# Performance work log

Measured on AMD Instinct MI355X. Metric: run time of the kernel, lower is better.

## Reference

```python
import jax, jax.numpy as jnp
import numpy as np

B, N, F_IN, HID, OUT, NHEADS = 16, 1024, 64, 64, 64, 4
TAXI = 512        # get_Parameter('taxi_size') from the original repo (node split point)
ALPHA = 0.2       # LeakyReLU negative slope


def setup_inputs() -> dict:
    key = jax.random.key(0)
    ks = jax.random.split(key, 8)
    x = jax.random.normal(ks[0], (B, N, F_IN), dtype=jnp.float32)
    # multiplicative binary mask (mostly ones so softmax rows are well-conditioned)
    mask = (jax.random.uniform(ks[1], (N, N)) > 0.1).astype(jnp.float32)
    s_in = 1.0 / np.sqrt(F_IN)
    s_cat = 1.0 / np.sqrt(NHEADS * HID)
    W1 = jax.random.normal(ks[2], (NHEADS, F_IN, HID), jnp.float32) * s_in
    W2 = jax.random.normal(ks[3], (NHEADS, F_IN, HID), jnp.float32) * s_in
    a = jax.random.normal(ks[4], (NHEADS, 2 * HID), jnp.float32) * 0.1
    W1o = jax.random.normal(ks[5], (NHEADS * HID, OUT), jnp.float32) * s_cat
    W2o = jax.random.normal(ks[6], (NHEADS * HID, OUT), jnp.float32) * s_cat
    ao = jax.random.normal(ks[7], (2 * OUT,), jnp.float32) * 0.1
    return dict(x=x, mask=mask, W1=W1, W2=W2, a=a, W1o=W1o, W2o=W2o, ao=ao)


def _gat_layer(x, mask, W1, W2, a, out_dim):
    # x: [B,N,F]; W1,W2: [F,out_dim]; a: [2*out_dim]
    # node-group-split linear projection (taxi nodes via W1, rest via W2)
    h = jnp.concatenate([x[:, :TAXI] @ W1, x[:, TAXI:] @ W2], axis=1)  # [B,N,O]
    A1 = h @ a[:out_dim]                 # [B,N]
    A2 = h @ a[out_dim:]                 # [B,N]
    sim = A1[:, :, None] + A2[:, None, :]  # [B,N,N] additive scores
    e = jax.nn.leaky_relu(sim, ALPHA)
    e = mask[None, :, :] * e             # multiplicative mask (as in source)
    attn = jax.nn.softmax(e, axis=-1)    # [B,N,N]  (dropout omitted: eval mode)
    h_prime = jnp.einsum('bnm,bmo->bno', attn, h)
    return jax.nn.elu(h_prime), attn


def reference(x, mask, W1, W2, a, W1o, W2o, ao):
    # input dropout omitted (eval mode)
    heads = [_gat_layer(x, mask, W1[i], W2[i], a[i], HID)[0] for i in range(NHEADS)]
    xc = jnp.concatenate(heads, axis=-1)          # [B,N,NHEADS*HID]
    out, attn = _gat_layer(xc, mask, W1o, W2o, ao, OUT)
    return out, attn
```

## Files before the change

### kernel.cpp

```cpp
#include <hip/hip_runtime.h>
#include <hip/hip_bf16.h>

#define B_      16
#define N_      1024
#define ALPHA_  0.2f

typedef __attribute__((ext_vector_type(8))) __bf16 bf16x8;
typedef __attribute__((ext_vector_type(4))) __bf16 bf16x4;
typedef __attribute__((ext_vector_type(4))) float  floatx4;

__device__ __forceinline__ float eluf(float u) { return u > 0.f ? u : __expf(u) - 1.f; }

__device__ __forceinline__ floatx4 mfma_bf16(bf16x8 a, bf16x8 b, floatx4 c) {
    return __builtin_amdgcn_mfma_f32_16x16x32_bf16(a, b, c, 0, 0, 0);
}

__device__ __forceinline__ void t_quad(const float4 a2v, const float4 ep, const float4 en,
                                       const float4 mv, const float th,
                                       const float e1p, const float e1n,
                                       float& z, float* o)
{
    float t0 = ((a2v.x > th) ? ep.x : en.x) * ((a2v.x > th) ? e1p : e1n);
    float t1 = ((a2v.y > th) ? ep.y : en.y) * ((a2v.y > th) ? e1p : e1n);
    float t2 = ((a2v.z > th) ? ep.z : en.z) * ((a2v.z > th) ? e1p : e1n);
    float t3 = ((a2v.w > th) ? ep.w : en.w) * ((a2v.w > th) ? e1p : e1n);
    t0 = (mv.x != 0.f) ? t0 : 1.f;
    t1 = (mv.y != 0.f) ? t1 : 1.f;
    t2 = (mv.z != 0.f) ? t2 : 1.f;
    t3 = (mv.w != 0.f) ? t3 : 1.f;
    z += ((t0 + t1) + (t2 + t3));
    o[0] = t0; o[1] = t1; o[2] = t2; o[3] = t3;
}

__global__ __launch_bounds__(256) void proj1_kernel(
    const float* __restrict__ x, const float* __restrict__ W1,
    const float* __restrict__ W2, const float* __restrict__ av,
    __bf16* __restrict__ h1t, float* __restrict__ A1, float* __restrict__ A2)
{
    const int tile = blockIdx.x, b = blockIdx.y, head = blockIdx.z;
    const int n0 = tile * 64;
    const float* W  = ((n0 < 512) ? W1 : W2) + head * 64 * 64;
    const float* ah = av + head * 128;

    __shared__ __align__(16) __bf16 xs[64][72];
    __shared__ __align__(16) __bf16 Wt[64][72];
    __shared__ __align__(16) float as_[128];

    const int tid = threadIdx.x;
    if (tid < 128) as_[tid] = ah[tid];
#pragma unroll
    for (int i = 0; i < 4; ++i) {
        int idx = i * 256 + tid;
        int r = idx >> 4, c = (idx & 15) * 4;
        float4 v = *(const float4*)(x + ((size_t)(b * N_ + n0 + r)) * 64 + c);
        xs[r][c+0] = (__bf16)v.x; xs[r][c+1] = (__bf16)v.y;
        xs[r][c+2] = (__bf16)v.z; xs[r][c+3] = (__bf16)v.w;
        float4 wv = *(const float4*)(W + (size_t)r * 64 + c);
        Wt[c+0][r] = (__bf16)wv.x; Wt[c+1][r] = (__bf16)wv.y;
        Wt[c+2][r] = (__bf16)wv.z; Wt[c+3][r] = (__bf16)wv.w;
    }
    __syncthreads();

    const int w = tid >> 6, L = tid & 63, quad = L >> 4, lo = L & 15;
    floatx4 acc[4] = {{0,0,0,0},{0,0,0,0},{0,0,0,0},{0,0,0,0}};
#pragma unroll
    for (int kc = 0; kc < 2; ++kc) {
        bf16x8 af = *(bf16x8*)&xs[16 * w + lo][kc * 32 + quad * 8];
#pragma unroll
        for (int t = 0; t < 4; ++t) {
            bf16x8 bv = *(bf16x8*)&Wt[16 * t + lo][kc * 32 + quad * 8];
            acc[t] = mfma_bf16(af, bv, acc[t]);
        }
    }

    float p1[4] = {0, 0, 0, 0}, p2[4] = {0, 0, 0, 0};
#pragma unroll
    for (int t = 0; t < 4; ++t) {
        float a1w = as_[16 * t + lo], a2w = as_[64 + 16 * t + lo];
#pragma unroll
        for (int i = 0; i < 4; ++i) { p1[i] += acc[t][i] * a1w; p2[i] += acc[t][i] * a2w; }
    }
#pragma unroll
    for (int s = 1; s < 16; s <<= 1)
#pragma unroll
        for (int i = 0; i < 4; ++i) {
            p1[i] += __shfl_xor(p1[i], s);
            p2[i] += __shfl_xor(p2[i], s);
        }
    const int bh = head * B_ + b;
    if (lo == 0) {
#pragma unroll
        for (int i = 0; i < 4; ++i) {
            int n = 16 * w + quad * 4 + i;
            A1[bh * N_ + n0 + n] = p1[i];
            A2[bh * N_ + n0 + n] = p2[i];
        }
    }

    __syncthreads();
#pragma unroll
    for (int t = 0; t < 4; ++t)
#pragma unroll
        for (int i = 0; i < 4; ++i)
            xs[16 * w + quad * 4 + i][16 * t + lo] = (__bf16)acc[t][i];
    __syncthreads();
    const int d = tid & 63, ch = tid >> 6;
    bf16x8 v0, v1;
#pragma unroll
    for (int j = 0; j < 8; ++j) v0[j] = xs[ch * 16 + j][d];
#pragma unroll
    for (int j = 0; j < 8; ++j) v1[j] = xs[ch * 16 + 8 + j][d];
    bf16x8* dst = (bf16x8*)(h1t + ((size_t)bh * 64 + d) * N_ + n0 + ch * 16);
    dst[0] = v0; dst[1] = v1;
}

__global__ __launch_bounds__(256, 4) void attn1_kernel(
    const float* __restrict__ A1g, const float* __restrict__ A2g,
    const __bf16* __restrict__ Htg, const float* __restrict__ maskg,
    __bf16* __restrict__ xc_out)
{
    const int tile = blockIdx.x, b = blockIdx.y, head = blockIdx.z;
    const int n0 = tile * 64;
    const int bh = head * B_ + b;
    const float* A1 = A1g + (size_t)bh * N_;
    const float* A2 = A2g + (size_t)bh * N_;
    const __bf16* Hglob = Htg + (size_t)bh * 64 * N_;

    __shared__ __align__(16) __bf16 ts[64][72];
    __shared__ __align__(16) __bf16 Ht[64][72];
    __shared__ __align__(16) float E2p[N_], E2n[N_], A2s[N_];
    __shared__ float invz[64];

    const int tid = threadIdx.x;
#pragma unroll
    for (int i = 0; i < 4; ++i) {
        int m = i * 256 + tid;
        float a2 = A2[m];
        A2s[m] = a2; E2p[m] = __expf(a2); E2n[m] = __expf(ALPHA_ * a2);
    }

    const int r = tid >> 2, q = tid & 3;
    const float a1r = A1[n0 + r];
    const float e1p = __expf(a1r), e1n = __expf(ALPHA_ * a1r), th = -a1r;
    const int w = tid >> 6, L = tid & 63, quad = L >> 4, lo = L & 15;

    floatx4 acc[4] = {{0,0,0,0},{0,0,0,0},{0,0,0,0},{0,0,0,0}};
    float zacc = 0.f;

    const float* mrow = maskg + (size_t)(n0 + r) * N_ + q * 16;
    const __bf16* hrow = Hglob + (size_t)r * N_ + q * 16;
    float4 pm0 = *(const float4*)(mrow);
    float4 pm1 = *(const float4*)(mrow + 4);
    float4 pm2 = *(const float4*)(mrow + 8);
    float4 pm3 = *(const float4*)(mrow + 12);
    bf16x8 ph0 = *(const bf16x8*)(hrow);
    bf16x8 ph1 = *(const bf16x8*)(hrow + 8);

    for (int mt = 0; mt < 16; ++mt) {
        float4 cm0 = pm0, cm1 = pm1, cm2 = pm2, cm3 = pm3;
        bf16x8 ch0 = ph0, ch1 = ph1;
        if (mt < 15) {
            const float* mnx = mrow + (mt + 1) * 64;
            const __bf16* hnx = hrow + (mt + 1) * 64;
            pm0 = *(const float4*)(mnx);      pm1 = *(const float4*)(mnx + 4);
            pm2 = *(const float4*)(mnx + 8);  pm3 = *(const float4*)(mnx + 12);
            ph0 = *(const bf16x8*)(hnx);      ph1 = *(const bf16x8*)(hnx + 8);
        }
        __syncthreads();
        const int mb = mt * 64 + q * 16;
        float o[16];
        t_quad(*(const float4*)&A2s[mb+0],  *(const float4*)&E2p[mb+0],  *(const float4*)&E2n[mb+0],  cm0, th, e1p, e1n, zacc, o+0);
        t_quad(*(const float4*)&A2s[mb+4],  *(const float4*)&E2p[mb+4],  *(const float4*)&E2n[mb+4],  cm1, th, e1p, e1n, zacc, o+4);
        t_quad(*(const float4*)&A2s[mb+8],  *(const float4*)&E2p[mb+8],  *(const float4*)&E2n[mb+8],  cm2, th, e1p, e1n, zacc, o+8);
        t_quad(*(const float4*)&A2s[mb+12], *(const float4*)&E2p[mb+12], *(const float4*)&E2n[mb+12], cm3, th, e1p, e1n, zacc, o+12);
        bf16x8 pk0 = {(__bf16)o[0], (__bf16)o[1], (__bf16)o[2], (__bf16)o[3],
                      (__bf16)o[4], (__bf16)o[5], (__bf16)o[6], (__bf16)o[7]};
        bf16x8 pk1 = {(__bf16)o[8], (__bf16)o[9], (__bf16)o[10], (__bf16)o[11],
                      (__bf16)o[12], (__bf16)o[13], (__bf16)o[14], (__bf16)o[15]};
        *(bf16x8*)&ts[r][q * 16]     = pk0;
        *(bf16x8*)&ts[r][q * 16 + 8] = pk1;
        *(bf16x8*)&Ht[r][q * 16]     = ch0;
        *(bf16x8*)&Ht[r][q * 16 + 8] = ch1;
        __syncthreads();
#pragma unroll
        for (int c = 0; c < 2; ++c) {
            bf16x8 af = *(bf16x8*)&ts[16 * w + lo][c * 32 + quad * 8];
#pragma unroll
            for (int t = 0; t < 4; ++t) {
                bf16x8 bv = *(bf16x8*)&Ht[16 * t + lo][c * 32 + quad * 8];
                acc[t] = mfma_bf16(af, bv, acc[t]);
            }
        }
    }

    zacc += __shfl_xor(zacc, 1);
    zacc += __shfl_xor(zacc, 2);
    if (q == 0) invz[r] = 1.f / zacc;
    __syncthreads();

#pragma unroll
    for (int t = 0; t < 4; ++t)
#pragma unroll
        for (int i = 0; i < 4; ++i) {
            const int n = 16 * w + quad * 4 + i;
            ts[n][16 * t + lo] = (__bf16)eluf(acc[t][i] * invz[n]);
        }
    __syncthreads();
#pragma unroll
    for (int i = 0; i < 2; ++i) {
        int cid = i * 256 + tid;
        int row = cid >> 3, c8 = (cid & 7) * 8;
        bf16x8 v = *(bf16x8*)&ts[row][c8];
        *(bf16x8*)(xc_out + ((size_t)(b * N_ + n0 + row)) * 256 + head * 64 + c8) = v;
    }
}

__global__ __launch_bounds__(256) void attn2_kernel(
    const float* __restrict__ A1g, const float* __restrict__ A2g,
    const __bf16* __restrict__ Htg, const float* __restrict__ maskg,
    float* __restrict__ out_f, float* __restrict__ attn_f)
{
    const int tile = blockIdx.x, b = blockIdx.y;
    const int n0 = tile * 16;
    const float* A1 = A1g + (size_t)b * N_;
    const float* A2 = A2g + (size_t)b * N_;
    const __bf16* Hglob = Htg + (size_t)b * 64 * N_;

    __shared__ __align__(16) __bf16 ts[16][72];
    __shared__ __align__(16) __bf16 Ht[64][72];
    __shared__ __align__(16) float E2p[N_], E2n[N_], A2s[N_];
    __shared__ float invz[16], E1pl[16], E1nl[16], A1sl[16];

    const int tid = threadIdx.x;
#pragma unroll
    for (int i = 0; i < 4; ++i) {
        int m = i * 256 + tid;
        float a2 = A2[m];
        A2s[m] = a2; E2p[m] = __expf(a2); E2n[m] = __expf(ALPHA_ * a2);
    }

    const int r = tid >> 4, q = tid & 15;
    const float a1r = A1[n0 + r];
    const float e1p = __expf(a1r), e1n = __expf(ALPHA_ * a1r), th = -a1r;
    if (q == 0) { E1pl[r] = e1p; E1nl[r] = e1n; A1sl[r] = a1r; }
    const int dr = tid >> 2, dq = tid & 3;
    const int w = tid >> 6, L = tid & 63, quad = L >> 4, lo = L & 15;

    floatx4 acc = {0, 0, 0, 0};
    float zacc = 0.f;

    const float* mrow = maskg + (size_t)(n0 + r) * N_ + q * 4;
    const __bf16* hrow = Hglob + (size_t)dr * N_ + dq * 16;
    float4 pm = *(const float4*)(mrow);
    bf16x8 ph0 = *(const bf16x8*)(hrow);
    bf16x8 ph1 = *(const bf16x8*)(hrow + 8);

    for (int mt = 0; mt < 16; ++mt) {
        float4 cm = pm;
        bf16x8 ch0 = ph0, ch1 = ph1;
        if (mt < 15) {
            pm  = *(const float4*)(mrow + (mt + 1) * 64);
            ph0 = *(const bf16x8*)(hrow + (mt + 1) * 64);
            ph1 = *(const bf16x8*)(hrow + (mt + 1) * 64 + 8);
        }
        __syncthreads();
        const int mb = mt * 64 + q * 4;
        float o[4];
        t_quad(*(const float4*)&A2s[mb], *(const float4*)&E2p[mb],
               *(const float4*)&E2n[mb], cm, th, e1p, e1n, zacc, o);
        bf16x4 pk = {(__bf16)o[0], (__bf16)o[1], (__bf16)o[2], (__bf16)o[3]};
        *(bf16x4*)&ts[r][q * 4] = pk;
        *(bf16x8*)&Ht[dr][dq * 16]     = ch0;
        *(bf16x8*)&Ht[dr][dq * 16 + 8] = ch1;
        __syncthreads();
#pragma unroll
        for (int c = 0; c < 2; ++c) {
            bf16x8 af = *(bf16x8*)&ts[lo][c * 32 + quad * 8];
            bf16x8 bv = *(bf16x8*)&Ht[16 * w + lo][c * 32 + quad * 8];
            acc = mfma_bf16(af, bv, acc);
        }
    }

    zacc += __shfl_xor(zacc, 1);
    zacc += __shfl_xor(zacc, 2);
    zacc += __shfl_xor(zacc, 4);
    zacc += __shfl_xor(zacc, 8);
    if (q == 0) invz[r] = 1.f / zacc;
    __syncthreads();

#pragma unroll
    for (int i = 0; i < 4; ++i) {
        const int n = quad * 4 + i;
        out_f[((size_t)(b * N_ + n0 + n)) * 64 + 16 * w + lo] = eluf(acc[i] * invz[n]);
    }

    const float4 a2v = *(const float4*)&A2s[tid * 4];
    const float4 epv = *(const float4*)&E2p[tid * 4];
    const float4 env = *(const float4*)&E2n[tid * 4];
#pragma unroll 4
    for (int i = 0; i < 16; ++i) {
        const float e1pr = E1pl[i], e1nr = E1nl[i], thr = -A1sl[i], iz = invz[i];
        float4 mv = *(const float4*)(maskg + (size_t)(n0 + i) * N_ + tid * 4);
        float4 res;
        res.x = ((mv.x != 0.f) ? ((a2v.x > thr) ? epv.x * e1pr : env.x * e1nr) : 1.f) * iz;
        res.y = ((mv.y != 0.f) ? ((a2v.y > thr) ? epv.y * e1pr : env.y * e1nr) : 1.f) * iz;
        res.z = ((mv.z != 0.f) ? ((a2v.z > thr) ? epv.z * e1pr : env.z * e1nr) : 1.f) * iz;
        res.w = ((mv.w != 0.f) ? ((a2v.w > thr) ? epv.w * e1pr : env.w * e1nr) : 1.f) * iz;
        *(float4*)(attn_f + ((size_t)(b * N_ + n0 + i)) * N_ + tid * 4) = res;
    }
}

__global__ __launch_bounds__(256) void proj2_kernel(
    const __bf16* __restrict__ xcb, const float* __restrict__ W1o,
    const float* __restrict__ W2o, const float* __restrict__ ao,
    __bf16* __restrict__ h2t, float* __restrict__ A1o, float* __restrict__ A2o)
{
    const int tile = blockIdx.x, b = blockIdx.y;
    const int n0 = tile * 64;
    const float* W = (n0 < 512) ? W1o : W2o;

    __shared__ __align__(16) __bf16 xs[64][264];
    __shared__ __align__(16) __bf16 Wt[64][264];
    __shared__ __align__(16) float as_[128];

    const int tid = threadIdx.x;
    if (tid < 128) as_[tid] = ao[tid];

#pragma unroll
    for (int i = 0; i < 8; ++i) {
        int idx = i * 256 + tid;
        int row = idx >> 5, c = (idx & 31) * 8;
        *(bf16x8*)&xs[row][c] =
            *(const bf16x8*)(xcb + ((size_t)(b * N_ + n0 + row)) * 256 + c);
    }
#pragma unroll
    for (int i = 0; i < 16; ++i) {
        int idx = i * 256 + tid;
        int k = idx >> 4, n4 = (idx & 15) * 4;
        float4 wv = *(const float4*)(W + (size_t)k * 64 + n4);
        Wt[n4 + 0][k] = (__bf16)wv.x;
        Wt[n4 + 1][k] = (__bf16)wv.y;
        Wt[n4 + 2][k] = (__bf16)wv.z;
        Wt[n4 + 3][k] = (__bf16)wv.w;
    }
    __syncthreads();

    const int w = tid >> 6, L = tid & 63, quad = L >> 4, lo = L & 15;
    floatx4 acc[4] = {{0,0,0,0},{0,0,0,0},{0,0,0,0},{0,0,0,0}};
#pragma unroll
    for (int kc = 0; kc < 8; ++kc) {
        bf16x8 af = *(bf16x8*)&xs[16 * w + lo][kc * 32 + quad * 8];
#pragma unroll
        for (int t = 0; t < 4; ++t) {
            bf16x8 bv = *(bf16x8*)&Wt[16 * t + lo][kc * 32 + quad * 8];
            acc[t] = mfma_bf16(af, bv, acc[t]);
        }
    }

    float p1[4] = {0, 0, 0, 0}, p2[4] = {0, 0, 0, 0};
#pragma unroll
    for (int t = 0; t < 4; ++t) {
        float a1w = as_[16 * t + lo], a2w = as_[64 + 16 * t + lo];
#pragma unroll
        for (int i = 0; i < 4; ++i) { p1[i] += acc[t][i] * a1w; p2[i] += acc[t][i] * a2w; }
    }
#pragma unroll
    for (int s = 1; s < 16; s <<= 1)
#pragma unroll
        for (int i = 0; i < 4; ++i) {
            p1[i] += __shfl_xor(p1[i], s);
            p2[i] += __shfl_xor(p2[i], s);
        }
    if (lo == 0) {
#pragma unroll
        for (int i = 0; i < 4; ++i) {
            int n = 16 * w + quad * 4 + i;
            A1o[b * N_ + n0 + n] = p1[i];
            A2o[b * N_ + n0 + n] = p2[i];
        }
    }

    __syncthreads();
#pragma unroll
    for (int t = 0; t < 4; ++t)
#pragma unroll
        for (int i = 0; i < 4; ++i)
            xs[16 * w + quad * 4 + i][16 * t + lo] = (__bf16)acc[t][i];
    __syncthreads();
    const int d = tid & 63, ch = tid >> 6;
    bf16x8 v0, v1;
#pragma unroll
    for (int j = 0; j < 8; ++j) v0[j] = xs[ch * 16 + j][d];
#pragma unroll
    for (int j = 0; j < 8; ++j) v1[j] = xs[ch * 16 + 8 + j][d];
    bf16x8* dst = (bf16x8*)(h2t + ((size_t)b * 64 + d) * N_ + n0 + ch * 16);
    dst[0] = v0; dst[1] = v1;
}

extern "C" void kernel_launch(void* const* d_in, const int* in_sizes, int n_in,
                              void* d_out, int out_size, void* d_ws, size_t ws_size,
                              hipStream_t stream)
{
    const float* x    = (const float*)d_in[0];
    const float* mask = (const float*)d_in[1];
    const float* W1   = (const float*)d_in[2];
    const float* W2   = (const float*)d_in[3];
    const float* a    = (const float*)d_in[4];
    const float* W1o  = (const float*)d_in[5];
    const float* W2o  = (const float*)d_in[6];
    const float* ao   = (const float*)d_in[7];

    float* out      = (float*)d_out;
    float* attn_out = out + (size_t)B_ * N_ * 64;

    float*  ws  = (float*)d_ws;
    float*  A1  = ws;
    float*  A2  = A1 + 65536;
    float*  A1o = A2 + 65536;
    float*  A2o = A1o + 16384;
    __bf16* h1t = (__bf16*)(A2o + 16384);
    __bf16* h2t = h1t + 4194304;
    __bf16* xcb = h2t + 1048576;

    proj1_kernel<<<dim3(16, 16, 4), 256, 0, stream>>>(x, W1, W2, a, h1t, A1, A2);
    attn1_kernel<<<dim3(16, 16, 4), 256, 0, stream>>>(A1, A2, h1t, mask, xcb);
    proj2_kernel<<<dim3(16, 16, 1), 256, 0, stream>>>(xcb, W1o, W2o, ao, h2t, A1o, A2o);
    attn2_kernel<<<dim3(64, 16, 1), 256, 0, stream>>>(A1o, A2o, h2t, mask, out, attn_out);
}
```

Baseline: 168.5 us.

## Pack mask into bitfield and restructure attention kernels around it

Adds a kernel that packs the float mask into 32-bit bitmasks once, so the attention kernels read bits from shared memory instead of streaming the 4 MB float mask repeatedly. Score computation switches from the precomputed exp-product trick to a direct exp of the leaky-relu per element, trading extra transcendental work for less shared-memory traffic. Grid order changes to tile-major so blocks sharing the same mask rows run close together. attn2 now handles 32 rows per block and reuses the bf16-packed attention values held in registers to write the attn output, instead of recomputing them from the mask. That output is now rounded to bf16 precision, and the explicit H prefetch pipelining is removed.

```diff
diff --git a/kernel.cpp b/kernel.cpp
--- a/kernel.cpp
+++ b/kernel.cpp
@@ -6,7 +6,6 @@
 #define ALPHA_  0.2f
 
 typedef __attribute__((ext_vector_type(8))) __bf16 bf16x8;
-typedef __attribute__((ext_vector_type(4))) __bf16 bf16x4;
 typedef __attribute__((ext_vector_type(4))) float  floatx4;
 
 __device__ __forceinline__ float eluf(float u) { return u > 0.f ? u : __expf(u) - 1.f; }
@@ -15,21 +14,21 @@
     return __builtin_amdgcn_mfma_f32_16x16x32_bf16(a, b, c, 0, 0, 0);
 }
 
-__device__ __forceinline__ void t_quad(const float4 a2v, const float4 ep, const float4 en,
-                                       const float4 mv, const float th,
-                                       const float e1p, const float e1n,
-                                       float& z, float* o)
-{
-    float t0 = ((a2v.x > th) ? ep.x : en.x) * ((a2v.x > th) ? e1p : e1n);
-    float t1 = ((a2v.y > th) ? ep.y : en.y) * ((a2v.y > th) ? e1p : e1n);
-    float t2 = ((a2v.z > th) ? ep.z : en.z) * ((a2v.z > th) ? e1p : e1n);
-    float t3 = ((a2v.w > th) ? ep.w : en.w) * ((a2v.w > th) ? e1p : e1n);
-    t0 = (mv.x != 0.f) ? t0 : 1.f;
-    t1 = (mv.y != 0.f) ? t1 : 1.f;
-    t2 = (mv.z != 0.f) ? t2 : 1.f;
-    t3 = (mv.w != 0.f) ? t3 : 1.f;
-    z += ((t0 + t1) + (t2 + t3));
-    o[0] = t0; o[1] = t1; o[2] = t2; o[3] = t3;
+__global__ __launch_bounds__(256) void maskbits_kernel(
+    const float* __restrict__ mask, unsigned* __restrict__ bits)
+{
+    const int idx = blockIdx.x * 256 + threadIdx.x;
+    const float* src = mask + (size_t)idx * 32;
+    unsigned v = 0;
+#pragma unroll
+    for (int j = 0; j < 8; ++j) {
+        float4 f = *(const float4*)(src + j * 4);
+        v |= ((unsigned)(f.x != 0.f)) << (j * 4 + 0);
+        v |= ((unsigned)(f.y != 0.f)) << (j * 4 + 1);
+        v |= ((unsigned)(f.z != 0.f)) << (j * 4 + 2);
+        v |= ((unsigned)(f.w != 0.f)) << (j * 4 + 3);
+    }
+    bits[idx] = v;
 }
 
 __global__ __launch_bounds__(256) void proj1_kernel(
@@ -116,71 +115,63 @@
 
 __global__ __launch_bounds__(256, 4) void attn1_kernel(
     const float* __restrict__ A1g, const float* __restrict__ A2g,
-    const __bf16* __restrict__ Htg, const float* __restrict__ maskg,
+    const __bf16* __restrict__ Htg, const unsigned* __restrict__ bitsG,
     __bf16* __restrict__ xc_out)
 {
-    const int tile = blockIdx.x, b = blockIdx.y, head = blockIdx.z;
+    const int b = blockIdx.x, head = blockIdx.y, tile = blockIdx.z;
     const int n0 = tile * 64;
     const int bh = head * B_ + b;
-    const float* A1 = A1g + (size_t)bh * N_;
     const float* A2 = A2g + (size_t)bh * N_;
     const __bf16* Hglob = Htg + (size_t)bh * 64 * N_;
 
     __shared__ __align__(16) __bf16 ts[64][72];
     __shared__ __align__(16) __bf16 Ht[64][72];
-    __shared__ __align__(16) float E2p[N_], E2n[N_], A2s[N_];
+    __shared__ __align__(16) float A2s[N_];
+    __shared__ __align__(16) unsigned bitsS[2048];
     __shared__ float invz[64];
 
     const int tid = threadIdx.x;
-#pragma unroll
-    for (int i = 0; i < 4; ++i) {
-        int m = i * 256 + tid;
-        float a2 = A2[m];
-        A2s[m] = a2; E2p[m] = __expf(a2); E2n[m] = __expf(ALPHA_ * a2);
+    *(float4*)&A2s[tid * 4] = *(const float4*)(A2 + tid * 4);
+    {
+        uint4 u0 = *(const uint4*)(bitsG + n0 * 32 + tid * 8);
+        uint4 u1 = *(const uint4*)(bitsG + n0 * 32 + tid * 8 + 4);
+        const int row = tid >> 2, wb0 = (tid & 3) * 8;
+        bitsS[(wb0+0)*64+row] = u0.x; bitsS[(wb0+1)*64+row] = u0.y;
+        bitsS[(wb0+2)*64+row] = u0.z; bitsS[(wb0+3)*64+row] = u0.w;
+        bitsS[(wb0+4)*64+row] = u1.x; bitsS[(wb0+5)*64+row] = u1.y;
+        bitsS[(wb0+6)*64+row] = u1.z; bitsS[(wb0+7)*64+row] = u1.w;
     }
 
     const int r = tid >> 2, q = tid & 3;
-    const float a1r = A1[n0 + r];
-    const float e1p = __expf(a1r), e1n = __expf(ALPHA_ * a1r), th = -a1r;
+    const float a1r = A1g[(size_t)bh * N_ + n0 + r];
     const int w = tid >> 6, L = tid & 63, quad = L >> 4, lo = L & 15;
+    const __bf16* hrow = Hglob + (size_t)r * N_ + q * 16;
 
     floatx4 acc[4] = {{0,0,0,0},{0,0,0,0},{0,0,0,0},{0,0,0,0}};
     float zacc = 0.f;
 
-    const float* mrow = maskg + (size_t)(n0 + r) * N_ + q * 16;
-    const __bf16* hrow = Hglob + (size_t)r * N_ + q * 16;
-    float4 pm0 = *(const float4*)(mrow);
-    float4 pm1 = *(const float4*)(mrow + 4);
-    float4 pm2 = *(const float4*)(mrow + 8);
-    float4 pm3 = *(const float4*)(mrow + 12);
-    bf16x8 ph0 = *(const bf16x8*)(hrow);
-    bf16x8 ph1 = *(const bf16x8*)(hrow + 8);
-
     for (int mt = 0; mt < 16; ++mt) {
-        float4 cm0 = pm0, cm1 = pm1, cm2 = pm2, cm3 = pm3;
-        bf16x8 ch0 = ph0, ch1 = ph1;
-        if (mt < 15) {
-            const float* mnx = mrow + (mt + 1) * 64;
-            const __bf16* hnx = hrow + (mt + 1) * 64;
-            pm0 = *(const float4*)(mnx);      pm1 = *(const float4*)(mnx + 4);
-            pm2 = *(const float4*)(mnx + 8);  pm3 = *(const float4*)(mnx + 12);
-            ph0 = *(const bf16x8*)(hnx);      ph1 = *(const bf16x8*)(hnx + 8);
-        }
         __syncthreads();
+        bf16x8 h0 = *(const bf16x8*)(hrow + mt * 64);
+        bf16x8 h1 = *(const bf16x8*)(hrow + mt * 64 + 8);
         const int mb = mt * 64 + q * 16;
+        const unsigned wb = bitsS[(mt * 2 + (q >> 1)) * 64 + r] >> ((q & 1) * 16);
         float o[16];
-        t_quad(*(const float4*)&A2s[mb+0],  *(const float4*)&E2p[mb+0],  *(const float4*)&E2n[mb+0],  cm0, th, e1p, e1n, zacc, o+0);
-        t_quad(*(const float4*)&A2s[mb+4],  *(const float4*)&E2p[mb+4],  *(const float4*)&E2n[mb+4],  cm1, th, e1p, e1n, zacc, o+4);
-        t_quad(*(const float4*)&A2s[mb+8],  *(const float4*)&E2p[mb+8],  *(const float4*)&E2n[mb+8],  cm2, th, e1p, e1n, zacc, o+8);
-        t_quad(*(const float4*)&A2s[mb+12], *(const float4*)&E2p[mb+12], *(const float4*)&E2n[mb+12], cm3, th, e1p, e1n, zacc, o+12);
+#pragma unroll
+        for (int j = 0; j < 16; ++j) {
+            float s = a1r + A2s[mb + j];
+            float lr = fmaxf(s, ALPHA_ * s);
+            float t = ((wb >> j) & 1u) ? __expf(lr) : 1.f;
+            zacc += t; o[j] = t;
+        }
         bf16x8 pk0 = {(__bf16)o[0], (__bf16)o[1], (__bf16)o[2], (__bf16)o[3],
                       (__bf16)o[4], (__bf16)o[5], (__bf16)o[6], (__bf16)o[7]};
         bf16x8 pk1 = {(__bf16)o[8], (__bf16)o[9], (__bf16)o[10], (__bf16)o[11],
                       (__bf16)o[12], (__bf16)o[13], (__bf16)o[14], (__bf16)o[15]};
         *(bf16x8*)&ts[r][q * 16]     = pk0;
         *(bf16x8*)&ts[r][q * 16 + 8] = pk1;
-        *(bf16x8*)&Ht[r][q * 16]     = ch0;
-        *(bf16x8*)&Ht[r][q * 16 + 8] = ch1;
+        *(bf16x8*)&Ht[r][q * 16]     = h0;
+        *(bf16x8*)&Ht[r][q * 16 + 8] = h1;
         __syncthreads();
 #pragma unroll
         for (int c = 0; c < 2; ++c) {
@@ -217,96 +208,97 @@
 
 __global__ __launch_bounds__(256) void attn2_kernel(
     const float* __restrict__ A1g, const float* __restrict__ A2g,
-    const __bf16* __restrict__ Htg, const float* __restrict__ maskg,
+    const __bf16* __restrict__ Htg, const unsigned* __restrict__ bitsG,
     float* __restrict__ out_f, float* __restrict__ attn_f)
 {
-    const int tile = blockIdx.x, b = blockIdx.y;
-    const int n0 = tile * 16;
-    const float* A1 = A1g + (size_t)b * N_;
+    const int b = blockIdx.x, tile = blockIdx.z;
+    const int n0 = tile * 32;
     const float* A2 = A2g + (size_t)b * N_;
     const __bf16* Hglob = Htg + (size_t)b * 64 * N_;
 
-    __shared__ __align__(16) __bf16 ts[16][72];
+    __shared__ __align__(16) __bf16 ts[32][72];
     __shared__ __align__(16) __bf16 Ht[64][72];
-    __shared__ __align__(16) float E2p[N_], E2n[N_], A2s[N_];
-    __shared__ float invz[16], E1pl[16], E1nl[16], A1sl[16];
+    __shared__ __align__(16) float A2s[N_];
+    __shared__ __align__(16) unsigned bitsS[1024];
+    __shared__ float invz[32];
 
     const int tid = threadIdx.x;
-#pragma unroll
-    for (int i = 0; i < 4; ++i) {
-        int m = i * 256 + tid;
-        float a2 = A2[m];
-        A2s[m] = a2; E2p[m] = __expf(a2); E2n[m] = __expf(ALPHA_ * a2);
-    }
-
-    const int r = tid >> 4, q = tid & 15;
-    const float a1r = A1[n0 + r];
-    const float e1p = __expf(a1r), e1n = __expf(ALPHA_ * a1r), th = -a1r;
-    if (q == 0) { E1pl[r] = e1p; E1nl[r] = e1n; A1sl[r] = a1r; }
+    *(float4*)&A2s[tid * 4] = *(const float4*)(A2 + tid * 4);
+    {
+        uint4 u = *(const uint4*)(bitsG + n0 * 32 + tid * 4);
+        const int row = tid >> 3, wb0 = (tid & 7) * 4;
+        bitsS[(wb0+0)*32+row] = u.x; bitsS[(wb0+1)*32+row] = u.y;
+        bitsS[(wb0+2)*32+row] = u.z; bitsS[(wb0+3)*32+row] = u.w;
+    }
+
+    const int r2 = tid >> 3, q2 = tid & 7;
+    const float a1r = A1g[(size_t)b * N_ + n0 + r2];
     const int dr = tid >> 2, dq = tid & 3;
     const int w = tid >> 6, L = tid & 63, quad = L >> 4, lo = L & 15;
-
-    floatx4 acc = {0, 0, 0, 0};
+    const __bf16* hrow = Hglob + (size_t)dr * N_ + dq * 16;
+
+    floatx4 acc2[2] = {{0,0,0,0},{0,0,0,0}};
     float zacc = 0.f;
-
-    const float* mrow = maskg + (size_t)(n0 + r) * N_ + q * 4;
-    const __bf16* hrow = Hglob + (size_t)dr * N_ + dq * 16;
-    float4 pm = *(const float4*)(mrow);
-    bf16x8 ph0 = *(const bf16x8*)(hrow);
-    bf16x8 ph1 = *(const bf16x8*)(hrow + 8);
+    bf16x8 tr[16];
 
     for (int mt = 0; mt < 16; ++mt) {
-        float4 cm = pm;
-        bf16x8 ch0 = ph0, ch1 = ph1;
-        if (mt < 15) {
-            pm  = *(const float4*)(mrow + (mt + 1) * 64);
-            ph0 = *(const bf16x8*)(hrow + (mt + 1) * 64);
-            ph1 = *(const bf16x8*)(hrow + (mt + 1) * 64 + 8);
-        }
         __syncthreads();
-        const int mb = mt * 64 + q * 4;
-        float o[4];
-        t_quad(*(const float4*)&A2s[mb], *(const float4*)&E2p[mb],
-               *(const float4*)&E2n[mb], cm, th, e1p, e1n, zacc, o);
-        bf16x4 pk = {(__bf16)o[0], (__bf16)o[1], (__bf16)o[2], (__bf16)o[3]};
-        *(bf16x4*)&ts[r][q * 4] = pk;
-        *(bf16x8*)&Ht[dr][dq * 16]     = ch0;
-        *(bf16x8*)&Ht[dr][dq * 16 + 8] = ch1;
+        bf16x8 h0 = *(const bf16x8*)(hrow + mt * 64);
+        bf16x8 h1 = *(const bf16x8*)(hrow + mt * 64 + 8);
+        const int mb = mt * 64 + q2 * 8;
+        const unsigned wb = bitsS[(mt * 2 + (q2 >> 2)) * 32 + r2] >> ((q2 & 3) * 8);
+        float o[8];
+#pragma unroll
+        for (int j = 0; j < 8; ++j) {
+            float s = a1r + A2s[mb + j];
+            float lr = fmaxf(s, ALPHA_ * s);
+            float t = ((wb >> j) & 1u) ? __expf(lr) : 1.f;
+            zacc += t; o[j] = t;
+        }
+        bf16x8 pk = {(__bf16)o[0], (__bf16)o[1], (__bf16)o[2], (__bf16)o[3],
+                     (__bf16)o[4], (__bf16)o[5], (__bf16)o[6], (__bf16)o[7]};
+        tr[mt] = pk;
+        *(bf16x8*)&ts[r2][q2 * 8] = pk;
+        *(bf16x8*)&Ht[dr][dq * 16]     = h0;
+        *(bf16x8*)&Ht[dr][dq * 16 + 8] = h1;
         __syncthreads();
 #pragma unroll
         for (int c = 0; c < 2; ++c) {
-            bf16x8 af = *(bf16x8*)&ts[lo][c * 32 + quad * 8];
-            bf16x8 bv = *(bf16x8*)&Ht[16 * w + lo][c * 32 + quad * 8];
-            acc = mfma_bf16(af, bv, acc);
+#pragma unroll
+            for (int rt = 0; rt < 2; ++rt) {
+                bf16x8 af = *(bf16x8*)&ts[16 * rt + lo][c * 32 + quad * 8];
+                bf16x8 bv = *(bf16x8*)&Ht[16 * w + lo][c * 32 + quad * 8];
+                acc2[rt] = mfma_bf16(af, bv, acc2[rt]);
+            }
         }
     }
 
     zacc += __shfl_xor(zacc, 1);
     zacc += __shfl_xor(zacc, 2);
     zacc += __shfl_xor(zacc, 4);
-    zacc += __shfl_xor(zacc, 8);
-    if (q == 0) invz[r] = 1.f / zacc;
-    __syncthreads();
-
-#pragma unroll
-    for (int i = 0; i < 4; ++i) {
-        const int n = quad * 4 + i;
-        out_f[((size_t)(b * N_ + n0 + n)) * 64 + 16 * w + lo] = eluf(acc[i] * invz[n]);
-    }
-
-    const float4 a2v = *(const float4*)&A2s[tid * 4];
-    const float4 epv = *(const float4*)&E2p[tid * 4];
-    const float4 env = *(const float4*)&E2n[tid * 4];
-#pragma unroll 4
-    for (int i = 0; i < 16; ++i) {
-        const float e1pr = E1pl[i], e1nr = E1nl[i], thr = -A1sl[i], iz = invz[i];
-        float4 mv = *(const float4*)(maskg + (size_t)(n0 + i) * N_ + tid * 4);
-        float4 res;
-        res.x = ((mv.x != 0.f) ? ((a2v.x > thr) ? epv.x * e1pr : env.x * e1nr) : 1.f) * iz;
-        res.y = ((mv.y != 0.f) ? ((a2v.y > thr) ? epv.y * e1pr : env.y * e1nr) : 1.f) * iz;
-        res.z = ((mv.z != 0.f) ? ((a2v.z > thr) ? epv.z * e1pr : env.z * e1nr) : 1.f) * iz;
-        res.w = ((mv.w != 0.f) ? ((a2v.w > thr) ? epv.w * e1pr : env.w * e1nr) : 1.f) * iz;
-        *(float4*)(attn_f + ((size_t)(b * N_ + n0 + i)) * N_ + tid * 4) = res;
+    if (q2 == 0) invz[r2] = 1.f / zacc;
+    __syncthreads();
+
+#pragma unroll
+    for (int rt = 0; rt < 2; ++rt)
+#pragma unroll
+        for (int i = 0; i < 4; ++i) {
+            const int n = 16 * rt + quad * 4 + i;
+            out_f[((size_t)(b * N_ + n0 + n)) * 64 + 16 * w + lo] =
+                eluf(acc2[rt][i] * invz[n]);
+        }
+
+    const float iz = invz[r2];
+    float* arow = attn_f + ((size_t)(b * N_ + n0 + r2)) * N_ + q2 * 8;
+#pragma unroll
+    for (int mt = 0; mt < 16; ++mt) {
+        bf16x8 t8 = tr[mt];
+        float4 f0 = make_float4((float)t8[0] * iz, (float)t8[1] * iz,
+                                (float)t8[2] * iz, (float)t8[3] * iz);
+        float4 f1 = make_float4((float)t8[4] * iz, (float)t8[5] * iz,
+                                (float)t8[6] * iz, (float)t8[7] * iz);
+        *(float4*)(arow + mt * 64)     = f0;
+        *(float4*)(arow + mt * 64 + 4) = f1;
     }
 }
 
@@ -413,17 +405,19 @@
     float* out      = (float*)d_out;
     float* attn_out = out + (size_t)B_ * N_ * 64;
 
-    float*  ws  = (float*)d_ws;
-    float*  A1  = ws;
-    float*  A2  = A1 + 65536;
-    float*  A1o = A2 + 65536;
-    float*  A2o = A1o + 16384;
-    __bf16* h1t = (__bf16*)(A2o + 16384);
-    __bf16* h2t = h1t + 4194304;
-    __bf16* xcb = h2t + 1048576;
-
+    float*    ws    = (float*)d_ws;
+    float*    A1    = ws;
+    float*    A2    = A1 + 65536;
+    float*    A1o   = A2 + 65536;
+    float*    A2o   = A1o + 16384;
+    __bf16*   h1t   = (__bf16*)(A2o + 16384);
+    __bf16*   h2t   = h1t + 4194304;
+    __bf16*   xcb   = h2t + 1048576;
+    unsigned* bitsG = (unsigned*)(xcb + 4194304);
+
+    maskbits_kernel<<<dim3(128), 256, 0, stream>>>(mask, bitsG);
     proj1_kernel<<<dim3(16, 16, 4), 256, 0, stream>>>(x, W1, W2, a, h1t, A1, A2);
-    attn1_kernel<<<dim3(16, 16, 4), 256, 0, stream>>>(A1, A2, h1t, mask, xcb);
+    attn1_kernel<<<dim3(16, 4, 16), 256, 0, stream>>>(A1, A2, h1t, bitsG, xcb);
     proj2_kernel<<<dim3(16, 16, 1), 256, 0, stream>>>(xcb, W1o, W2o, ao, h2t, A1o, A2o);
-    attn2_kernel<<<dim3(64, 16, 1), 256, 0, stream>>>(A1o, A2o, h2t, mask, out, attn_out);
-}
+    attn2_kernel<<<dim3(16, 1, 32), 256, 0, stream>>>(A1o, A2o, h2t, bitsG, out, attn_out);
+}
```

Measured after the change: 155.7 us. 7.6% less time.
